# Optimization experiments

Hardware: AMD Instinct MI355X
Metric: run time of the kernel (lower is better)

## Reference

```python
import jax, jax.numpy as jnp
import numpy as np

N_NODES = 100000
N_EDGES = 6400000
D = 12

def setup_inputs() -> dict:
    key = jax.random.key(0)
    k1, k2, k3, k4 = jax.random.split(key, 4)
    x = jax.random.normal(k1, (N_NODES, D), dtype=jnp.float32)
    W_l = jax.random.normal(k2, (D, D), dtype=jnp.float32) / np.sqrt(D)
    W_r = jax.random.normal(k3, (D, D), dtype=jnp.float32) / np.sqrt(D)
    b = jnp.zeros((D,), dtype=jnp.float32)
    edge_index = jax.random.randint(k4, (2, N_EDGES), 0, N_NODES, dtype=jnp.int64)
    return {"x": x, "W_l": W_l, "W_r": W_r, "b": b, "edge_index": edge_index}

def reference(x, W_l, W_r, b, edge_index):
    # PyG SAGEConv (mean aggregation): out = lin_l(mean_{j in N(i)} x_j) + lin_r(x_i)
    src = edge_index[0]
    dst = edge_index[1]
    n = x.shape[0]
    msgs = x[src]                                      # [E, D] gather
    agg = jax.ops.segment_sum(msgs, dst, num_segments=n)          # [N, D]
    cnt = jax.ops.segment_sum(jnp.ones_like(dst, dtype=x.dtype), dst, num_segments=n)
    mean = agg / jnp.maximum(cnt, 1.0)[:, None]        # [N, D]
    out = mean @ W_l.T + x @ W_r.T + b                 # lin_l carries the bias in PyG
    return out
```

## Files before the change

### kernel.cpp

```cpp
#include <hip/hip_runtime.h>

#define N_NODES 100000
#define N_EDGES 6400000
#define D 12

#define SLOG 7
#define SSZ  128
#define NB   ((N_NODES + SSZ - 1) / SSZ)
#define SBLK 256
#define STHR 512
#define SEPB (N_EDGES / SBLK)
#define CAPS 64
#define OVMAX 65536

#define CHUNK 1792
#define SPT   7

#define NBLK 512
#define EPB  ((N_EDGES + NBLK - 1) / NBLK)
#define CAP4 2048
#define EPT4 (CAP4 / 256)

__device__ __forceinline__ unsigned int f2bf(float f) {
    unsigned int u = __float_as_uint(f);
    return (u + 0x7fffu + ((u >> 16) & 1u)) >> 16;
}
__device__ __forceinline__ unsigned int pk2(float lo, float hi) {
    return (f2bf(hi) << 16) | f2bf(lo);
}
__device__ __forceinline__ float bflo(unsigned int u) { return __uint_as_float(u << 16); }
__device__ __forceinline__ float bfhi(unsigned int u) { return __uint_as_float(u & 0xffff0000u); }

__global__ __launch_bounds__(256) void prep_kernel(
    const float* __restrict__ x, unsigned int* __restrict__ xb, int* ovctr)
{
    int i = blockIdx.x * 256 + threadIdx.x;
    if (i == 0 && ovctr) *ovctr = 0;
    if (i >= N_NODES) return;
    const float4* xr = (const float4*)(x) + (size_t)i * 3;
    float4 a = xr[0], b = xr[1], c = xr[2];
    unsigned int* o = xb + (size_t)i * 8;
    ((uint4*)o)[0] = make_uint4(pk2(a.x, a.y), pk2(a.z, a.w), pk2(b.x, b.y), pk2(b.z, b.w));
    ((uint2*)(o + 4))[0] = make_uint2(pk2(c.x, c.y), pk2(c.z, c.w));
}

__global__ __launch_bounds__(512) void scatter1_kernel(
    const int* __restrict__ ei, unsigned int* __restrict__ strip,
    int* __restrict__ cnt, uint2* __restrict__ ovbuf, int* __restrict__ ovctr)
{
    __shared__ int cur[NB];
    int t = threadIdx.x;
    int b = blockIdx.x;
    for (int i = t; i < NB; i += STHR) cur[i] = 0;
    __syncthreads();

    const int* dei = ei + N_EDGES;
    int start = b * SEPB;
    int end = start + SEPB;

    int e = start + t;
    while (e + 3 * STHR < end) {
        int s0 = ei[e], s1 = ei[e + STHR], s2 = ei[e + 2 * STHR], s3 = ei[e + 3 * STHR];
        int d0 = dei[e], d1 = dei[e + STHR], d2 = dei[e + 2 * STHR], d3 = dei[e + 3 * STHR];
        int k0 = d0 >> SLOG, k1 = d1 >> SLOG, k2 = d2 >> SLOG, k3 = d3 >> SLOG;
        int p0 = atomicAdd(&cur[k0], 1);
        int p1 = atomicAdd(&cur[k1], 1);
        int p2 = atomicAdd(&cur[k2], 1);
        int p3 = atomicAdd(&cur[k3], 1);
        if (p0 < CAPS) strip[((size_t)(k0 * SBLK + b)) * CAPS + p0] = ((unsigned)s0 << SLOG) | (unsigned)(d0 & (SSZ - 1));
        else { int ix = atomicAdd(ovctr, 1); if (ix < OVMAX) ovbuf[ix] = make_uint2((unsigned)s0, (unsigned)d0); }
        if (p1 < CAPS) strip[((size_t)(k1 * SBLK + b)) * CAPS + p1] = ((unsigned)s1 << SLOG) | (unsigned)(d1 & (SSZ - 1));
        else { int ix = atomicAdd(ovctr, 1); if (ix < OVMAX) ovbuf[ix] = make_uint2((unsigned)s1, (unsigned)d1); }
        if (p2 < CAPS) strip[((size_t)(k2 * SBLK + b)) * CAPS + p2] = ((unsigned)s2 << SLOG) | (unsigned)(d2 & (SSZ - 1));
        else { int ix = atomicAdd(ovctr, 1); if (ix < OVMAX) ovbuf[ix] = make_uint2((unsigned)s2, (unsigned)d2); }
        if (p3 < CAPS) strip[((size_t)(k3 * SBLK + b)) * CAPS + p3] = ((unsigned)s3 << SLOG) | (unsigned)(d3 & (SSZ - 1));
        else { int ix = atomicAdd(ovctr, 1); if (ix < OVMAX) ovbuf[ix] = make_uint2((unsigned)s3, (unsigned)d3); }
        e += 4 * STHR;
    }
    while (e < end) {
        int s = ei[e], d = dei[e];
        int k = d >> SLOG;
        int p = atomicAdd(&cur[k], 1);
        if (p < CAPS) strip[((size_t)(k * SBLK + b)) * CAPS + p] = ((unsigned)s << SLOG) | (unsigned)(d & (SSZ - 1));
        else { int ix = atomicAdd(ovctr, 1); if (ix < OVMAX) ovbuf[ix] = make_uint2((unsigned)s, (unsigned)d); }
        e += STHR;
    }
    __syncthreads();
    int* crow = cnt + (size_t)b * NB;
    for (int i = t; i < NB; i += STHR) crow[i] = cur[i];
}

__global__ __launch_bounds__(256) void agg_strip_kernel(
    const unsigned int* __restrict__ strip, const int* __restrict__ cntm,
    const uint2* __restrict__ ovbuf, const int* __restrict__ ovctr,
    const unsigned int* __restrict__ xb,
    const float* __restrict__ x, const float* __restrict__ Wl,
    const float* __restrict__ Wr, const float* __restrict__ bias,
    float* __restrict__ out)
{
    __shared__ float sWl[D * D], sWr[D * D], sb[D];
    __shared__ int cnt[SSZ];
    __shared__ int sbuf[SSZ];
    __shared__ int segbase[SSZ + 1];
    __shared__ int cursor[SSZ];
    __shared__ int cnt_tot[SSZ];
    __shared__ int seglen[SBLK];
    __shared__ unsigned vals[CHUNK * 6];

    int t = threadIdx.x;
    int k = blockIdx.x;

    if (t < D * D) { sWl[t] = Wl[t]; sWr[t] = Wr[t]; }
    if (t < D) sb[t] = bias[t];
    if (t < SSZ) cnt_tot[t] = 0;

    if (t < SBLK) {
        int c = cntm[(size_t)t * NB + k];
        seglen[t] = c < CAPS ? c : CAPS;
    }
    __syncthreads();

    float acc[D];
#pragma unroll
    for (int d = 0; d < D; ++d) acc[d] = 0.f;

    int loc = t >> 1;
    int sub = t & 1;

    const unsigned int* kstrip = strip + (size_t)k * SBLK * CAPS;

    const int TOTS = SBLK * CAPS;
    for (int c0 = 0; c0 < TOTS; c0 += CHUNK) {
        int n = min(CHUNK, TOTS - c0);
        if (t < SSZ) cnt[t] = 0;
        __syncthreads();

        unsigned pe[SPT];
        bool va[SPT];
#pragma unroll
        for (int q = 0; q < SPT; ++q) {
            int j = t + 256 * q;
            int v = c0 + j;
            bool ok = j < n;
            int s = v >> 6;
            va[q] = ok && ((v & 63) < seglen[ok ? s : 0]);
            pe[q] = ok ? kstrip[v] : 0u;
        }
#pragma unroll
        for (int q = 0; q < SPT; ++q)
            if (va[q]) atomicAdd(&cnt[pe[q] & (SSZ - 1)], 1);
        __syncthreads();

        if (t < SSZ) sbuf[t] = cnt[t];
        __syncthreads();
        for (int o = 1; o < SSZ; o <<= 1) {
            int v = (t < SSZ && t >= o) ? sbuf[t - o] : 0;
            __syncthreads();
            if (t < SSZ) sbuf[t] += v;
            __syncthreads();
        }
        if (t < SSZ) {
            segbase[t + 1] = sbuf[t];
            if (t == 0) segbase[0] = 0;
        }
        __syncthreads();
        if (t < SSZ) { cursor[t] = segbase[t]; cnt_tot[t] += cnt[t]; }
        __syncthreads();

#pragma unroll
        for (int q = 0; q < SPT; ++q) {
            if (va[q]) {
                unsigned p = pe[q];
                int slot = atomicAdd(&cursor[p & (SSZ - 1)], 1);
                const unsigned* r = xb + (size_t)(p >> SLOG) * 8;
                uint2 q0 = ((const uint2*)r)[0];
                uint2 q1 = ((const uint2*)r)[1];
                uint2 q2 = ((const uint2*)r)[2];
                unsigned* vv = &vals[slot * 6];
                ((uint2*)vv)[0] = q0;
                ((uint2*)vv)[1] = q1;
                ((uint2*)vv)[2] = q2;
            }
        }
        __syncthreads();

        int a0 = segbase[loc], a1 = segbase[loc + 1];
        for (int j = a0 + sub; j < a1; j += 2) {
            const unsigned* vv = &vals[j * 6];
            uint2 q0 = ((const uint2*)vv)[0];
            uint2 q1 = ((const uint2*)vv)[1];
            uint2 q2 = ((const uint2*)vv)[2];
            acc[0]  += bflo(q0.x); acc[1]  += bfhi(q0.x);
            acc[2]  += bflo(q0.y); acc[3]  += bfhi(q0.y);
            acc[4]  += bflo(q1.x); acc[5]  += bfhi(q1.x);
            acc[6]  += bflo(q1.y); acc[7]  += bfhi(q1.y);
            acc[8]  += bflo(q2.x); acc[9]  += bfhi(q2.x);
            acc[10] += bflo(q2.y); acc[11] += bfhi(q2.y);
        }
        __syncthreads();
    }

    int novf = *ovctr;
    if (novf > OVMAX) novf = OVMAX;
    if (sub == 0 && novf > 0) {
        int matches = 0;
        for (int j = 0; j < novf; ++j) {
            uint2 eo = ovbuf[j];
            if ((int)(eo.y >> SLOG) == k && (int)(eo.y & (SSZ - 1)) == loc) {
                const unsigned* r = xb + (size_t)eo.x * 8;
                uint2 q0 = ((const uint2*)r)[0];
                uint2 q1 = ((const uint2*)r)[1];
                uint2 q2 = ((const uint2*)r)[2];
                acc[0]  += bflo(q0.x); acc[1]  += bfhi(q0.x);
                acc[2]  += bflo(q0.y); acc[3]  += bfhi(q0.y);
                acc[4]  += bflo(q1.x); acc[5]  += bfhi(q1.x);
                acc[6]  += bflo(q1.y); acc[7]  += bfhi(q1.y);
                acc[8]  += bflo(q2.x); acc[9]  += bfhi(q2.x);
                acc[10] += bflo(q2.y); acc[11] += bfhi(q2.y);
                ++matches;
            }
        }
        if (matches) atomicAdd(&cnt_tot[loc], matches);
    }

    float* red = (float*)vals;
#pragma unroll
    for (int d = 0; d < D; ++d) red[sub * 1664 + loc * 13 + d] = acc[d];
    __syncthreads();

    if (t < SSZ) {
        int node = k * SSZ + t;
        if (node < N_NODES) {
            float m[D];
#pragma unroll
            for (int d = 0; d < D; ++d)
                m[d] = red[t * 13 + d] + red[1664 + t * 13 + d];
            float inv = 1.f / fmaxf((float)cnt_tot[t], 1.f);
#pragma unroll
            for (int d = 0; d < D; ++d) m[d] *= inv;

            float xi[D];
            const float4* xr = (const float4*)(x) + (size_t)node * 3;
            float4 x0 = xr[0], x1 = xr[1], x2 = xr[2];
            xi[0] = x0.x; xi[1] = x0.y; xi[2]  = x0.z; xi[3]  = x0.w;
            xi[4] = x1.x; xi[5] = x1.y; xi[6]  = x1.z; xi[7]  = x1.w;
            xi[8] = x2.x; xi[9] = x2.y; xi[10] = x2.z; xi[11] = x2.w;

            float o[D];
#pragma unroll
            for (int oo = 0; oo < D; ++oo) {
                float a = sb[oo];
#pragma unroll
                for (int d = 0; d < D; ++d) {
                    a += m[d] * sWl[oo * D + d];
                    a += xi[d] * sWr[oo * D + d];
                }
                o[oo] = a;
            }
            float4* orow = (float4*)(out) + (size_t)node * 3;
            orow[0] = make_float4(o[0], o[1], o[2], o[3]);
            orow[1] = make_float4(o[4], o[5], o[6], o[7]);
            orow[2] = make_float4(o[8], o[9], o[10], o[11]);
        }
    }
}


__global__ __launch_bounds__(256) void hist_kernel(
    const int* __restrict__ ei, int* __restrict__ bins)
{
    __shared__ int h[NB];
    for (int i = threadIdx.x; i < NB; i += 256) h[i] = 0;
    __syncthreads();
    const int* dei = ei + N_EDGES;
    int start = blockIdx.x * EPB;
    int end = min(start + EPB, N_EDGES);
    int e = start + (int)threadIdx.x;
    while (e + 768 < end) {
        int d0 = dei[e], d1 = dei[e + 256], d2 = dei[e + 512], d3 = dei[e + 768];
        atomicAdd(&h[d0 >> SLOG], 1);
        atomicAdd(&h[d1 >> SLOG], 1);
        atomicAdd(&h[d2 >> SLOG], 1);
        atomicAdd(&h[d3 >> SLOG], 1);
        e += 1024;
    }
    while (e < end) { atomicAdd(&h[dei[e] >> SLOG], 1); e += 256; }
    __syncthreads();
    for (int i = threadIdx.x; i < NB; i += 256) {
        int c = h[i];
        if (c) atomicAdd(&bins[i], c);
    }
}

__global__ __launch_bounds__(1024) void scan_kernel(
    const int* __restrict__ bins, int* __restrict__ base, int* __restrict__ cursor)
{
    __shared__ int buf[1024];
    __shared__ int carry;
    int tid = threadIdx.x;
    if (tid == 0) carry = 0;
    __syncthreads();
    for (int c0 = 0; c0 < NB; c0 += 1024) {
        int i = c0 + tid;
        int v = (i < NB) ? bins[i] : 0;
        buf[tid] = v;
        __syncthreads();
        for (int o = 1; o < 1024; o <<= 1) {
            int t = (tid >= o) ? buf[tid - o] : 0;
            __syncthreads();
            buf[tid] += t;
            __syncthreads();
        }
        int excl = buf[tid] - v + carry;
        if (i < NB) { base[i] = excl; cursor[i] = excl; }
        __syncthreads();
        if (tid == 0) carry += buf[1023];
        __syncthreads();
    }
    if (tid == 0) base[NB] = N_EDGES;
}

__global__ __launch_bounds__(512) void scatter_sort_kernel(
    const int* __restrict__ ei, int* __restrict__ cursor,
    unsigned int* __restrict__ sorted)
{
    __shared__ int h[NB];
    for (int i = threadIdx.x; i < NB; i += STHR) h[i] = 0;
    __syncthreads();
    const int* dei = ei + N_EDGES;
    int start = blockIdx.x * SEPB;
    int end = min(start + SEPB, N_EDGES);
    int e = start + (int)threadIdx.x;
    while (e + 3 * STHR < end) {
        int d0 = dei[e], d1 = dei[e + STHR], d2 = dei[e + 2 * STHR], d3 = dei[e + 3 * STHR];
        atomicAdd(&h[d0 >> SLOG], 1);
        atomicAdd(&h[d1 >> SLOG], 1);
        atomicAdd(&h[d2 >> SLOG], 1);
        atomicAdd(&h[d3 >> SLOG], 1);
        e += 4 * STHR;
    }
    while (e < end) { atomicAdd(&h[dei[e] >> SLOG], 1); e += STHR; }
    __syncthreads();
    for (int i = threadIdx.x; i < NB; i += STHR) {
        int c = h[i];
        h[i] = c ? atomicAdd(&cursor[i], c) : 0;
    }
    __syncthreads();
    e = start + (int)threadIdx.x;
    while (e + 3 * STHR < end) {
        int s0 = ei[e], s1 = ei[e + STHR], s2 = ei[e + 2 * STHR], s3 = ei[e + 3 * STHR];
        int d0 = dei[e], d1 = dei[e + STHR], d2 = dei[e + 2 * STHR], d3 = dei[e + 3 * STHR];
        int p0 = atomicAdd(&h[d0 >> SLOG], 1);
        int p1 = atomicAdd(&h[d1 >> SLOG], 1);
        int p2 = atomicAdd(&h[d2 >> SLOG], 1);
        int p3 = atomicAdd(&h[d3 >> SLOG], 1);
        sorted[p0] = ((unsigned)s0 << SLOG) | (unsigned)(d0 & (SSZ - 1));
        sorted[p1] = ((unsigned)s1 << SLOG) | (unsigned)(d1 & (SSZ - 1));
        sorted[p2] = ((unsigned)s2 << SLOG) | (unsigned)(d2 & (SSZ - 1));
        sorted[p3] = ((unsigned)s3 << SLOG) | (unsigned)(d3 & (SSZ - 1));
        e += 4 * STHR;
    }
    while (e < end) {
        int s = ei[e], d = dei[e];
        int pos = atomicAdd(&h[d >> SLOG], 1);
        sorted[pos] = ((unsigned)s << SLOG) | (unsigned)(d & (SSZ - 1));
        e += STHR;
    }
}

__global__ __launch_bounds__(256) void agg_reg4_kernel(
    const unsigned int* __restrict__ sorted, const int* __restrict__ base,
    const unsigned int* __restrict__ xb,
    const float* __restrict__ x, const float* __restrict__ Wl,
    const float* __restrict__ Wr, const float* __restrict__ bias,
    float* __restrict__ out)
{
    __shared__ float sWl[D * D], sWr[D * D], sb[D];
    __shared__ int cnt[SSZ];
    __shared__ int sbuf[SSZ];
    __shared__ int segbase[SSZ + 1];
    __shared__ int cursor[SSZ];
    __shared__ int cnt_tot[SSZ];
    __shared__ unsigned vals[CAP4 * 6];

    int t = threadIdx.x;
    int b = blockIdx.x;

    if (t < D * D) { sWl[t] = Wl[t]; sWr[t] = Wr[t]; }
    if (t < D) sb[t] = bias[t];
    if (t < SSZ) cnt_tot[t] = 0;

    float acc[D];
#pragma unroll
    for (int d = 0; d < D; ++d) acc[d] = 0.f;

    int loc = t >> 1;
    int sub = t & 1;

    int start = base[b];
    int end = base[b + 1];

    for (int c0 = start; c0 < end; c0 += CAP4) {
        int n = min(CAP4, end - c0);
        if (t < SSZ) cnt[t] = 0;
        __syncthreads();

        unsigned pe[EPT4];
        int ne = 0;
        for (int j = t; j < n; j += 256) pe[ne++] = sorted[c0 + j];
#pragma unroll
        for (int q = 0; q < EPT4; ++q)
            if (q < ne) atomicAdd(&cnt[pe[q] & (SSZ - 1)], 1);
        __syncthreads();

        if (t < SSZ) sbuf[t] = cnt[t];
        __syncthreads();
        for (int o = 1; o < SSZ; o <<= 1) {
            int v = (t < SSZ && t >= o) ? sbuf[t - o] : 0;
            __syncthreads();
            if (t < SSZ) sbuf[t] += v;
            __syncthreads();
        }
        if (t < SSZ) {
            segbase[t + 1] = sbuf[t];
            if (t == 0) segbase[0] = 0;
        }
        __syncthreads();
        if (t < SSZ) { cursor[t] = segbase[t]; cnt_tot[t] += cnt[t]; }
        __syncthreads();

#pragma unroll
        for (int q = 0; q < EPT4; ++q) {
            if (q < ne) {
                unsigned p = pe[q];
                int slot = atomicAdd(&cursor[p & (SSZ - 1)], 1);
                const unsigned* r = xb + (size_t)(p >> SLOG) * 8;
                uint2 q0 = ((const uint2*)r)[0];
                uint2 q1 = ((const uint2*)r)[1];
                uint2 q2 = ((const uint2*)r)[2];
                unsigned* vv = &vals[slot * 6];
                ((uint2*)vv)[0] = q0;
                ((uint2*)vv)[1] = q1;
                ((uint2*)vv)[2] = q2;
            }
        }
        __syncthreads();

        int a0 = segbase[loc], a1 = segbase[loc + 1];
        for (int j = a0 + sub; j < a1; j += 2) {
            const unsigned* vv = &vals[j * 6];
            uint2 q0 = ((const uint2*)vv)[0];
            uint2 q1 = ((const uint2*)vv)[1];
            uint2 q2 = ((const uint2*)vv)[2];
            acc[0]  += bflo(q0.x); acc[1]  += bfhi(q0.x);
            acc[2]  += bflo(q0.y); acc[3]  += bfhi(q0.y);
            acc[4]  += bflo(q1.x); acc[5]  += bfhi(q1.x);
            acc[6]  += bflo(q1.y); acc[7]  += bfhi(q1.y);
            acc[8]  += bflo(q2.x); acc[9]  += bfhi(q2.x);
            acc[10] += bflo(q2.y); acc[11] += bfhi(q2.y);
        }
        __syncthreads();
    }

    float* red = (float*)vals;
#pragma unroll
    for (int d = 0; d < D; ++d) red[sub * 1664 + loc * 13 + d] = acc[d];
    __syncthreads();

    if (t < SSZ) {
        int node = b * SSZ + t;
        if (node < N_NODES) {
            float m[D];
#pragma unroll
            for (int d = 0; d < D; ++d)
                m[d] = red[t * 13 + d] + red[1664 + t * 13 + d];
            float inv = 1.f / fmaxf((float)cnt_tot[t], 1.f);
#pragma unroll
            for (int d = 0; d < D; ++d) m[d] *= inv;

            float xi[D];
            const float4* xr = (const float4*)(x) + (size_t)node * 3;
            float4 x0 = xr[0], x1 = xr[1], x2 = xr[2];
            xi[0] = x0.x; xi[1] = x0.y; xi[2]  = x0.z; xi[3]  = x0.w;
            xi[4] = x1.x; xi[5] = x1.y; xi[6]  = x1.z; xi[7]  = x1.w;
            xi[8] = x2.x; xi[9] = x2.y; xi[10] = x2.z; xi[11] = x2.w;

            float o[D];
#pragma unroll
            for (int oo = 0; oo < D; ++oo) {
                float a = sb[oo];
#pragma unroll
                for (int d = 0; d < D; ++d) {
                    a += m[d] * sWl[oo * D + d];
                    a += xi[d] * sWr[oo * D + d];
                }
                o[oo] = a;
            }
            float4* orow = (float4*)(out) + (size_t)node * 3;
            orow[0] = make_float4(o[0], o[1], o[2], o[3]);
            orow[1] = make_float4(o[4], o[5], o[6], o[7]);
            orow[2] = make_float4(o[8], o[9], o[10], o[11]);
        }
    }
}


__global__ __launch_bounds__(256) void scatter_kernel(
    const int* __restrict__ ei, const float* __restrict__ x,
    float* __restrict__ agg, float* __restrict__ cnt)
{
    int e = blockIdx.x * blockDim.x + threadIdx.x;
    if (e >= N_EDGES) return;
    int src = ei[e];
    int dst = ei[N_EDGES + e];
    const float4* xr = (const float4*)(x + (size_t)src * D);
    float4 a = xr[0], b4 = xr[1], c = xr[2];
    float* dr = agg + (size_t)dst * D;
    atomicAdd(dr + 0,  a.x);  atomicAdd(dr + 1,  a.y);
    atomicAdd(dr + 2,  a.z);  atomicAdd(dr + 3,  a.w);
    atomicAdd(dr + 4,  b4.x); atomicAdd(dr + 5,  b4.y);
    atomicAdd(dr + 6,  b4.z); atomicAdd(dr + 7,  b4.w);
    atomicAdd(dr + 8,  c.x);  atomicAdd(dr + 9,  c.y);
    atomicAdd(dr + 10, c.z);  atomicAdd(dr + 11, c.w);
    atomicAdd(cnt + dst, 1.0f);
}

__global__ __launch_bounds__(256) void finalize_kernel(
    const float* __restrict__ x, const float* __restrict__ Wl,
    const float* __restrict__ Wr, const float* __restrict__ bias,
    const float* __restrict__ agg, const float* __restrict__ cnt,
    float* __restrict__ out)
{
    __shared__ float sWl[D * D], sWr[D * D], sb[D];
    int t = threadIdx.x;
    if (t < D * D) { sWl[t] = Wl[t]; sWr[t] = Wr[t]; }
    if (t < D) sb[t] = bias[t];
    __syncthreads();
    int i = blockIdx.x * blockDim.x + t;
    if (i >= N_NODES) return;
    float inv = 1.0f / fmaxf(cnt[i], 1.0f);
    float m[D], xi[D];
    const float4* ar = (const float4*)(agg + (size_t)i * D);
    const float4* xr = (const float4*)(x + (size_t)i * D);
    float4 a0 = ar[0], a1 = ar[1], a2 = ar[2];
    float4 x0 = xr[0], x1 = xr[1], x2 = xr[2];
    m[0] = a0.x * inv; m[1] = a0.y * inv; m[2]  = a0.z * inv; m[3]  = a0.w * inv;
    m[4] = a1.x * inv; m[5] = a1.y * inv; m[6]  = a1.z * inv; m[7]  = a1.w * inv;
    m[8] = a2.x * inv; m[9] = a2.y * inv; m[10] = a2.z * inv; m[11] = a2.w * inv;
    xi[0] = x0.x; xi[1] = x0.y; xi[2]  = x0.z; xi[3]  = x0.w;
    xi[4] = x1.x; xi[5] = x1.y; xi[6]  = x1.z; xi[7]  = x1.w;
    xi[8] = x2.x; xi[9] = x2.y; xi[10] = x2.z; xi[11] = x2.w;
    float o[D];
#pragma unroll
    for (int oo = 0; oo < D; ++oo) {
        float acc = sb[oo];
#pragma unroll
        for (int d = 0; d < D; ++d) {
            acc += m[d] * sWl[oo * D + d];
            acc += xi[d] * sWr[oo * D + d];
        }
        o[oo] = acc;
    }
    float4* orow = (float4*)(out + (size_t)i * D);
    orow[0] = make_float4(o[0], o[1], o[2], o[3]);
    orow[1] = make_float4(o[4], o[5], o[6], o[7]);
    orow[2] = make_float4(o[8], o[9], o[10], o[11]);
}

extern "C" void kernel_launch(void* const* d_in, const int* in_sizes, int n_in,
                              void* d_out, int out_size, void* d_ws, size_t ws_size,
                              hipStream_t stream) {
    const float* x    = (const float*)d_in[0];
    const float* Wl   = (const float*)d_in[1];
    const float* Wr   = (const float*)d_in[2];
    const float* bias = (const float*)d_in[3];
    const int*   ei   = (const int*)d_in[4];
    float* out = (float*)d_out;

    size_t stripBytes  = (size_t)NB * SBLK * CAPS * sizeof(unsigned int);
    size_t xbBytes     = (size_t)N_NODES * 8 * sizeof(unsigned int);
    size_t cntBytes    = (size_t)SBLK * NB * sizeof(int);
    size_t ovBytes     = (size_t)OVMAX * sizeof(uint2);
    size_t neededNew   = stripBytes + xbBytes + cntBytes + ovBytes + 64;

    size_t sortedBytes = (size_t)N_EDGES * sizeof(unsigned int);
    size_t binsBytes   = (size_t)NB * sizeof(int);
    size_t baseBytes   = (size_t)(NB + 1) * sizeof(int);
    size_t neededMid   = sortedBytes + xbBytes + binsBytes + baseBytes + binsBytes;
    size_t neededLast  = ((size_t)N_NODES * D + N_NODES) * sizeof(float);

    if (ws_size >= neededNew) {
        char* p = (char*)d_ws;
        unsigned int* strip = (unsigned int*)p;         p += stripBytes;
        unsigned int* xb    = (unsigned int*)p;         p += xbBytes;
        int* cnt    = (int*)p;                          p += cntBytes;
        uint2* ovbuf = (uint2*)p;                       p += ovBytes;
        int* ovctr  = (int*)p;

        prep_kernel<<<(N_NODES + 255) / 256, 256, 0, stream>>>(x, xb, ovctr);
        scatter1_kernel<<<SBLK, STHR, 0, stream>>>(ei, strip, cnt, ovbuf, ovctr);
        agg_strip_kernel<<<NB, 256, 0, stream>>>(strip, cnt, ovbuf, ovctr, xb, x, Wl, Wr, bias, out);
    } else if (ws_size >= neededMid) {
        char* p = (char*)d_ws;
        unsigned int* sorted = (unsigned int*)p;        p += sortedBytes;
        unsigned int* xb     = (unsigned int*)p;        p += xbBytes;
        int* bins   = (int*)p;                          p += binsBytes;
        int* base   = (int*)p;                          p += baseBytes;
        int* cursor = (int*)p;

        hipMemsetAsync(bins, 0, binsBytes, stream);
        prep_kernel<<<(N_NODES + 255) / 256, 256, 0, stream>>>(x, xb, nullptr);
        hist_kernel<<<NBLK, 256, 0, stream>>>(ei, bins);
        scan_kernel<<<1, 1024, 0, stream>>>(bins, base, cursor);
        scatter_sort_kernel<<<SBLK, STHR, 0, stream>>>(ei, cursor, sorted);
        agg_reg4_kernel<<<NB, 256, 0, stream>>>(sorted, base, xb, x, Wl, Wr, bias, out);
    } else {
        float* agg = (float*)d_ws;
        float* cnt = agg + (size_t)N_NODES * D;
        hipMemsetAsync(d_ws, 0, neededLast, stream);
        scatter_kernel<<<(N_EDGES + 255) / 256, 256, 0, stream>>>(ei, x, agg, cnt);
        finalize_kernel<<<(N_NODES + 255) / 256, 256, 0, stream>>>(x, Wl, Wr, bias, agg, cnt, out);
    }
}
```

Baseline: 266.0 us.

## Shrink strip capacity, use wavefront shuffle scan, stage overflow edges in LDS

```diff
diff --git a/kernel.cpp b/kernel.cpp
--- a/kernel.cpp
+++ b/kernel.cpp
@@ -10,7 +10,7 @@
 #define SBLK 256
 #define STHR 512
 #define SEPB (N_EDGES / SBLK)
-#define CAPS 64
+#define CAPS 48
 #define OVMAX 65536
 
 #define CHUNK 1792
@@ -100,11 +100,11 @@
 {
     __shared__ float sWl[D * D], sWr[D * D], sb[D];
     __shared__ int cnt[SSZ];
-    __shared__ int sbuf[SSZ];
     __shared__ int segbase[SSZ + 1];
     __shared__ int cursor[SSZ];
     __shared__ int cnt_tot[SSZ];
     __shared__ int seglen[SBLK];
+    __shared__ uint2 ovstage[256];
     __shared__ unsigned vals[CHUNK * 6];
 
     int t = threadIdx.x;
@@ -142,8 +142,9 @@
             int j = t + 256 * q;
             int v = c0 + j;
             bool ok = j < n;
-            int s = v >> 6;
-            va[q] = ok && ((v & 63) < seglen[ok ? s : 0]);
+            int s = v / CAPS;
+            int r = v - s * CAPS;
+            va[q] = ok && (r < seglen[ok ? s : 0]);
             pe[q] = ok ? kstrip[v] : 0u;
         }
 #pragma unroll
@@ -151,16 +152,24 @@
             if (va[q]) atomicAdd(&cnt[pe[q] & (SSZ - 1)], 1);
         __syncthreads();
 
-        if (t < SSZ) sbuf[t] = cnt[t];
-        __syncthreads();
-        for (int o = 1; o < SSZ; o <<= 1) {
-            int v = (t < SSZ && t >= o) ? sbuf[t - o] : 0;
-            __syncthreads();
-            if (t < SSZ) sbuf[t] += v;
-            __syncthreads();
-        }
-        if (t < SSZ) {
-            segbase[t + 1] = sbuf[t];
+        if (t < 64) {
+            int a = cnt[t];
+            int bq = cnt[64 + t];
+            int ia = a;
+#pragma unroll
+            for (int dd = 1; dd < 64; dd <<= 1) {
+                int tmp = __shfl_up(ia, dd);
+                if (t >= dd) ia += tmp;
+            }
+            int tot_a = __shfl(ia, 63);
+            int ib = bq;
+#pragma unroll
+            for (int dd = 1; dd < 64; dd <<= 1) {
+                int tmp = __shfl_up(ib, dd);
+                if (t >= dd) ib += tmp;
+            }
+            segbase[t + 1] = ia;
+            segbase[65 + t] = ib + tot_a;
             if (t == 0) segbase[0] = 0;
         }
         __syncthreads();
@@ -202,25 +211,31 @@
 
     int novf = *ovctr;
     if (novf > OVMAX) novf = OVMAX;
-    if (sub == 0 && novf > 0) {
-        int matches = 0;
-        for (int j = 0; j < novf; ++j) {
-            uint2 eo = ovbuf[j];
-            if ((int)(eo.y >> SLOG) == k && (int)(eo.y & (SSZ - 1)) == loc) {
-                const unsigned* r = xb + (size_t)eo.x * 8;
-                uint2 q0 = ((const uint2*)r)[0];
-                uint2 q1 = ((const uint2*)r)[1];
-                uint2 q2 = ((const uint2*)r)[2];
-                acc[0]  += bflo(q0.x); acc[1]  += bfhi(q0.x);
-                acc[2]  += bflo(q0.y); acc[3]  += bfhi(q0.y);
-                acc[4]  += bflo(q1.x); acc[5]  += bfhi(q1.x);
-                acc[6]  += bflo(q1.y); acc[7]  += bfhi(q1.y);
-                acc[8]  += bflo(q2.x); acc[9]  += bfhi(q2.x);
-                acc[10] += bflo(q2.y); acc[11] += bfhi(q2.y);
-                ++matches;
+    for (int base = 0; base < novf; base += 256) {
+        int m = min(256, novf - base);
+        if (t < m) ovstage[t] = ovbuf[base + t];
+        __syncthreads();
+        if (sub == 0) {
+            int matches = 0;
+            for (int j = 0; j < m; ++j) {
+                uint2 eo = ovstage[j];
+                if ((int)(eo.y >> SLOG) == k && (int)(eo.y & (SSZ - 1)) == loc) {
+                    const unsigned* r = xb + (size_t)eo.x * 8;
+                    uint2 q0 = ((const uint2*)r)[0];
+                    uint2 q1 = ((const uint2*)r)[1];
+                    uint2 q2 = ((const uint2*)r)[2];
+                    acc[0]  += bflo(q0.x); acc[1]  += bfhi(q0.x);
+                    acc[2]  += bflo(q0.y); acc[3]  += bfhi(q0.y);
+                    acc[4]  += bflo(q1.x); acc[5]  += bfhi(q1.x);
+                    acc[6]  += bflo(q1.y); acc[7]  += bfhi(q1.y);
+                    acc[8]  += bflo(q2.x); acc[9]  += bfhi(q2.x);
+                    acc[10] += bflo(q2.y); acc[11] += bfhi(q2.y);
+                    ++matches;
+                }
             }
-        }
-        if (matches) atomicAdd(&cnt_tot[loc], matches);
+            if (matches) atomicAdd(&cnt_tot[loc], matches);
+        }
+        __syncthreads();
     }
 
     float* red = (float*)vals;
```

After: 445.0 us. +67.3%, slower.
